# Kernel tuning notes

Measured on AMD Instinct MI355X. Metric: run time of the kernel, lower is better.

## Reference

```python
import jax, jax.numpy as jnp
import numpy as np
from jax import lax

STRIDE = 1
PAD = 1  # module pads 1 on each side whenever padding != 0


def setup_inputs() -> dict:
    key = jax.random.key(0)
    kx, kw, kb = jax.random.split(key, 3)
    x = jax.random.normal(kx, (4096, 4096), dtype=jnp.float32)
    weight = jax.random.normal(kw, (15, 15), dtype=jnp.float32)
    bias = jax.random.normal(kb, (1,), dtype=jnp.float32)
    return {"x": x, "weight": weight, "bias": bias}


def reference(x, weight, bias):
    # Single-channel 2D cross-correlation with constant zero padding of 1 and
    # stride STRIDE, plus a scalar bias. lax.conv_general_dilated computes
    # correlation (no kernel flip), matching the torch corr2d loop exactly.
    out = lax.conv_general_dilated(
        x[None, None, :, :],          # NCHW, N=C=1
        weight[None, None, :, :],      # OIHW, O=I=1
        window_strides=(STRIDE, STRIDE),
        padding=[(PAD, PAD), (PAD, PAD)],
        dimension_numbers=("NCHW", "OIHW", "NCHW"),
    )[0, 0]
    return out + bias[0]
```

## Files before the change

kernel.cpp:

```cpp
#include <hip/hip_runtime.h>
#include <hip/hip_bf16.h>

#define IN_N   4096
#define OW     4084
#define KS     15
#define TILE   64
#define XROWS  78
#define XCOLS  80
#define XS     88

typedef __attribute__((ext_vector_type(8))) short v8s;
typedef __attribute__((ext_vector_type(4))) float v4f;

__device__ __forceinline__ unsigned short f2bf(float f) {
    union { float f; unsigned u; } c; c.f = f;
    unsigned r = c.u + 0x7fff + ((c.u >> 16) & 1);
    return (unsigned short)(r >> 16);
}

__global__ __launch_bounds__(256) void conv2d_mfma(
    const float* __restrict__ x, const float* __restrict__ w,
    const float* __restrict__ bias, float* __restrict__ out)
{
    __shared__ unsigned short xtile[XROWS * XS] __attribute__((aligned(16)));
    __shared__ unsigned short Bbuf[KS * 512]   __attribute__((aligned(16)));

    const int tid = threadIdx.x;
    const int X0 = blockIdx.x * TILE;
    const int Y0 = blockIdx.y * TILE;

    for (int p = tid; p < KS * 64; p += 256) {
        int ky = p >> 6, e = p & 63;
        int n = e & 15, quad = e >> 4;
        unsigned short vals[8];
        #pragma unroll
        for (int j = 0; j < 8; ++j) {
            int k = quad * 8 + j;
            int d = k - n;
            float wv = (d >= 0 && d < KS) ? w[ky * KS + d] : 0.0f;
            vals[j] = f2bf(wv);
        }
        *(v8s*)(&Bbuf[ky * 512 + e * 8]) = *(const v8s*)vals;
    }

    for (int p = tid; p < XROWS * (XCOLS / 2); p += 256) {
        int tr = p / (XCOLS / 2);
        int cp = p - tr * (XCOLS / 2);
        int gr = Y0 - 1 + tr;
        int gc = X0 - 1 + cp * 2;
        float f0 = 0.0f, f1 = 0.0f;
        if ((unsigned)gr < (unsigned)IN_N) {
            const float* xr = x + (size_t)gr * IN_N;
            if ((unsigned)gc       < (unsigned)IN_N) f0 = xr[gc];
            if ((unsigned)(gc + 1) < (unsigned)IN_N) f1 = xr[gc + 1];
        }
        unsigned pack = (unsigned)f2bf(f0) | ((unsigned)f2bf(f1) << 16);
        *(unsigned*)(&xtile[tr * XS + cp * 2]) = pack;
    }
    __syncthreads();

    const int lane = tid & 63;
    const int wv   = tid >> 6;
    const int m    = lane & 15;
    const int quad = lane >> 4;

    v4f acc[4];
    #pragma unroll
    for (int t = 0; t < 4; ++t) acc[t] = (v4f){0.f, 0.f, 0.f, 0.f};

    const int rowbase = wv * 16 + m;
    const int colbase = quad * 8;

    #pragma unroll 5
    for (int ky = 0; ky < KS; ++ky) {
        v8s bfrag = *(const v8s*)(&Bbuf[ky * 512 + lane * 8]);
        const unsigned short* arow = &xtile[(rowbase + ky) * XS + colbase];
        #pragma unroll
        for (int t = 0; t < 4; ++t) {
            v8s afrag = *(const v8s*)(arow + t * 16);
            acc[t] = __builtin_amdgcn_mfma_f32_16x16x32_bf16(afrag, bfrag, acc[t], 0, 0, 0);
        }
    }

    const float bv = bias[0];
    const int orow0 = Y0 + wv * 16 + quad * 4;
    const int ocol0 = X0 + (lane & 15);
    #pragma unroll
    for (int t = 0; t < 4; ++t) {
        int oc = ocol0 + t * 16;
        if (oc < OW) {
            #pragma unroll
            for (int r = 0; r < 4; ++r) {
                int orow = orow0 + r;
                if (orow < OW)
                    out[(size_t)orow * OW + oc] = acc[t][r] + bv;
            }
        }
    }
}

extern "C" void kernel_launch(void* const* d_in, const int* in_sizes, int n_in,
                              void* d_out, int out_size, void* d_ws, size_t ws_size,
                              hipStream_t stream) {
    const float* x    = (const float*)d_in[0];
    const float* w    = (const float*)d_in[1];
    const float* bias = (const float*)d_in[2];
    float* out        = (float*)d_out;

    dim3 grid((OW + TILE - 1) / TILE, (OW + TILE - 1) / TILE);
    conv2d_mfma<<<grid, dim3(256), 0, stream>>>(x, w, bias, out);
}
```

Baseline: 155.5 us.

## Hoist banded weight matrix into separate kernel and specialize interior tile loads

Builds the bf16 banded Toeplitz weight fragments once in a small pre-kernel written to workspace, instead of every block recomputing them into shared memory. The main kernel reads B fragments from global memory (cached) with a one-step prefetch, fully unrolls the ky loop, and uses a fixed 40x6 thread mapping to load the input tile with bounds checks skipped for interior blocks. Output stores also skip bounds checks for non-edge blocks, and launch bounds request 6 blocks per CU. This cuts per-block setup work and LDS usage, at the cost of an extra kernel launch and relying on the workspace buffer. Only 240 of 256 threads take part in the tile load.

```diff
diff --git a/kernel.cpp b/kernel.cpp
--- a/kernel.cpp
+++ b/kernel.cpp
@@ -1,5 +1,4 @@
 #include <hip/hip_runtime.h>
-#include <hip/hip_bf16.h>
 
 #define IN_N   4096
 #define OW     4084
@@ -8,6 +7,8 @@
 #define XROWS  78
 #define XCOLS  80
 #define XS     88
+#define NBX    64
+#define NBY    64
 
 typedef __attribute__((ext_vector_type(8))) short v8s;
 typedef __attribute__((ext_vector_type(4))) float v4f;
@@ -18,44 +19,60 @@
     return (unsigned short)(r >> 16);
 }
 
-__global__ __launch_bounds__(256) void conv2d_mfma(
-    const float* __restrict__ x, const float* __restrict__ w,
+__global__ void build_B(const float* __restrict__ w, unsigned short* __restrict__ Bg) {
+    int ky = blockIdx.x;
+    int e  = threadIdx.x;
+    int n = e & 15, quad = e >> 4;
+    unsigned short vals[8];
+    #pragma unroll
+    for (int j = 0; j < 8; ++j) {
+        int d = quad * 8 + j - n;
+        vals[j] = (d >= 0 && d < KS) ? f2bf(w[ky * KS + d]) : (unsigned short)0;
+    }
+    *(v8s*)(&Bg[(ky * 64 + e) * 8]) = *(const v8s*)vals;
+}
+
+__global__ __launch_bounds__(256, 6) void conv2d_mfma2(
+    const float* __restrict__ x, const unsigned short* __restrict__ Bg,
     const float* __restrict__ bias, float* __restrict__ out)
 {
     __shared__ unsigned short xtile[XROWS * XS] __attribute__((aligned(16)));
-    __shared__ unsigned short Bbuf[KS * 512]   __attribute__((aligned(16)));
 
     const int tid = threadIdx.x;
-    const int X0 = blockIdx.x * TILE;
-    const int Y0 = blockIdx.y * TILE;
+    const int bx = blockIdx.x, by = blockIdx.y;
+    const int X0 = bx * TILE;
+    const int Y0 = by * TILE;
 
-    for (int p = tid; p < KS * 64; p += 256) {
-        int ky = p >> 6, e = p & 63;
-        int n = e & 15, quad = e >> 4;
-        unsigned short vals[8];
-        #pragma unroll
-        for (int j = 0; j < 8; ++j) {
-            int k = quad * 8 + j;
-            int d = k - n;
-            float wv = (d >= 0 && d < KS) ? w[ky * KS + d] : 0.0f;
-            vals[j] = f2bf(wv);
+    const int tx = tid % 40;
+    const int ty = tid / 40;
+    const bool interior = (bx > 0) & (bx < NBX - 1) & (by > 0) & (by < NBY - 1);
+
+    if (ty < 6) {
+        unsigned short* dst = &xtile[ty * XS + 2 * tx];
+        if (interior) {
+            const float* xr = x + (size_t)(Y0 - 1 + ty) * IN_N + (X0 - 1 + 2 * tx);
+            #pragma unroll
+            for (int i = 0; i < 13; ++i) {
+                float f0 = xr[0], f1 = xr[1];
+                *(unsigned*)dst = (unsigned)f2bf(f0) | ((unsigned)f2bf(f1) << 16);
+                xr  += 6 * IN_N;
+                dst += 6 * XS;
+            }
+        } else {
+            const int gc0 = X0 - 1 + 2 * tx;
+            #pragma unroll
+            for (int i = 0; i < 13; ++i) {
+                int gr = Y0 - 1 + ty + 6 * i;
+                float f0 = 0.0f, f1 = 0.0f;
+                if ((unsigned)gr < (unsigned)IN_N) {
+                    const float* xr = x + (size_t)gr * IN_N;
+                    if ((unsigned)gc0       < (unsigned)IN_N) f0 = xr[gc0];
+                    if ((unsigned)(gc0 + 1) < (unsigned)IN_N) f1 = xr[gc0 + 1];
+                }
+                *(unsigned*)dst = (unsigned)f2bf(f0) | ((unsigned)f2bf(f1) << 16);
+                dst += 6 * XS;
+            }
         }
-        *(v8s*)(&Bbuf[ky * 512 + e * 8]) = *(const v8s*)vals;
-    }
-
-    for (int p = tid; p < XROWS * (XCOLS / 2); p += 256) {
-        int tr = p / (XCOLS / 2);
-        int cp = p - tr * (XCOLS / 2);
-        int gr = Y0 - 1 + tr;
-        int gc = X0 - 1 + cp * 2;
-        float f0 = 0.0f, f1 = 0.0f;
-        if ((unsigned)gr < (unsigned)IN_N) {
-            const float* xr = x + (size_t)gr * IN_N;
-            if ((unsigned)gc       < (unsigned)IN_N) f0 = xr[gc];
-            if ((unsigned)(gc + 1) < (unsigned)IN_N) f1 = xr[gc + 1];
-        }
-        unsigned pack = (unsigned)f2bf(f0) | ((unsigned)f2bf(f1) << 16);
-        *(unsigned*)(&xtile[tr * XS + cp * 2]) = pack;
     }
     __syncthreads();
 
@@ -68,32 +85,47 @@
     #pragma unroll
     for (int t = 0; t < 4; ++t) acc[t] = (v4f){0.f, 0.f, 0.f, 0.f};
 
-    const int rowbase = wv * 16 + m;
-    const int colbase = quad * 8;
+    const v8s* Bgv = (const v8s*)Bg;
+    v8s bcur = Bgv[lane];
+    const unsigned short* arow = &xtile[(wv * 16 + m) * XS + quad * 8];
 
-    #pragma unroll 5
+    #pragma unroll
     for (int ky = 0; ky < KS; ++ky) {
-        v8s bfrag = *(const v8s*)(&Bbuf[ky * 512 + lane * 8]);
-        const unsigned short* arow = &xtile[(rowbase + ky) * XS + colbase];
-        #pragma unroll
-        for (int t = 0; t < 4; ++t) {
-            v8s afrag = *(const v8s*)(arow + t * 16);
-            acc[t] = __builtin_amdgcn_mfma_f32_16x16x32_bf16(afrag, bfrag, acc[t], 0, 0, 0);
-        }
+        v8s bnext = (ky < KS - 1) ? Bgv[(ky + 1) * 64 + lane] : bcur;
+        v8s a0 = *(const v8s*)(arow + 0);
+        v8s a1 = *(const v8s*)(arow + 16);
+        v8s a2 = *(const v8s*)(arow + 32);
+        v8s a3 = *(const v8s*)(arow + 48);
+        acc[0] = __builtin_amdgcn_mfma_f32_16x16x32_bf16(a0, bcur, acc[0], 0, 0, 0);
+        acc[1] = __builtin_amdgcn_mfma_f32_16x16x32_bf16(a1, bcur, acc[1], 0, 0, 0);
+        acc[2] = __builtin_amdgcn_mfma_f32_16x16x32_bf16(a2, bcur, acc[2], 0, 0, 0);
+        acc[3] = __builtin_amdgcn_mfma_f32_16x16x32_bf16(a3, bcur, acc[3], 0, 0, 0);
+        arow += XS;
+        bcur = bnext;
     }
 
     const float bv = bias[0];
     const int orow0 = Y0 + wv * 16 + quad * 4;
-    const int ocol0 = X0 + (lane & 15);
-    #pragma unroll
-    for (int t = 0; t < 4; ++t) {
-        int oc = ocol0 + t * 16;
-        if (oc < OW) {
+    const int ocol0 = X0 + m;
+    if (interior | ((bx < NBX - 1) & (by < NBY - 1))) {
+        float* o0 = &out[(size_t)orow0 * OW + ocol0];
+        #pragma unroll
+        for (int t = 0; t < 4; ++t) {
             #pragma unroll
-            for (int r = 0; r < 4; ++r) {
-                int orow = orow0 + r;
-                if (orow < OW)
-                    out[(size_t)orow * OW + oc] = acc[t][r] + bv;
+            for (int r = 0; r < 4; ++r)
+                o0[(size_t)r * OW + t * 16] = acc[t][r] + bv;
+        }
+    } else {
+        #pragma unroll
+        for (int t = 0; t < 4; ++t) {
+            int oc = ocol0 + t * 16;
+            if (oc < OW) {
+                #pragma unroll
+                for (int r = 0; r < 4; ++r) {
+                    int orow = orow0 + r;
+                    if (orow < OW)
+                        out[(size_t)orow * OW + oc] = acc[t][r] + bv;
+                }
             }
         }
     }
@@ -106,7 +138,9 @@
     const float* w    = (const float*)d_in[1];
     const float* bias = (const float*)d_in[2];
     float* out        = (float*)d_out;
+    unsigned short* Bg = (unsigned short*)d_ws;
 
-    dim3 grid((OW + TILE - 1) / TILE, (OW + TILE - 1) / TILE);
-    conv2d_mfma<<<grid, dim3(256), 0, stream>>>(x, w, bias, out);
+    build_B<<<dim3(KS), dim3(64), 0, stream>>>(w, Bg);
+    dim3 grid(NBX, NBY);
+    conv2d_mfma2<<<grid, dim3(256), 0, stream>>>(x, Bg, bias, out);
 }
```

After: 136.4 us. -12.3%, faster.
